# Kernel optimization log

Hardware: AMD Instinct MI355X
Metric: run time of the kernel (lower is better)

Reference implementation:

```python
import jax, jax.numpy as jnp
import numpy as np

N_NODES = 100000


def setup_inputs() -> dict:
    key = jax.random.key(0)
    k1, k2, k3, k4, k5, k6 = jax.random.split(key, 6)
    x = jax.random.normal(k1, (N_NODES, 256), dtype=jnp.float32)
    edge_index = jax.random.randint(k2, (2, 3200000), 0, N_NODES, dtype=jnp.int64)
    # GCNConv(256, 3): glorot weight + zero bias (PyG default)
    lim1 = float(np.sqrt(6.0 / (256 + 3)))
    W1 = jax.random.uniform(k3, (256, 3), minval=-lim1, maxval=lim1, dtype=jnp.float32)
    b1 = jnp.zeros((3,), dtype=jnp.float32)
    # Linear(3, 7): torch default kaiming-uniform-ish bounds
    lim2 = float(1.0 / np.sqrt(3))
    W2 = jax.random.uniform(k4, (3, 7), minval=-lim2, maxval=lim2, dtype=jnp.float32)
    b2 = jax.random.uniform(k5, (7,), minval=-lim2, maxval=lim2, dtype=jnp.float32)
    return {"x": x, "edge_index": edge_index, "W1": W1, "b1": b1, "W2": W2, "b2": b2}


def gcn_conv(x, edge_index, W, b, num_nodes):
    # PyG GCNConv: add self-loops, symmetric deg^-1/2 (A+I) deg^-1/2 normalization,
    # aggregate transformed features, then add bias.
    loop = jnp.arange(num_nodes, dtype=edge_index.dtype)
    src = jnp.concatenate([edge_index[0], loop])
    dst = jnp.concatenate([edge_index[1], loop])
    ones = jnp.ones_like(dst, dtype=x.dtype)
    deg = jax.ops.segment_sum(ones, dst, num_segments=num_nodes)  # [N]
    dinv = jnp.where(deg > 0, jax.lax.rsqrt(deg), 0.0)
    norm = dinv[src] * dinv[dst]  # [E+N]
    h = x @ W  # [N, 3] — transform BEFORE gather (small width)
    msg = h[src] * norm[:, None]  # [E+N, 3]
    agg = jax.ops.segment_sum(msg, dst, num_segments=num_nodes)  # [N, 3]
    return agg + b


def reference(x, edge_index, W1, b1, W2, b2):
    h = jax.nn.relu(gcn_conv(x, edge_index, W1, b1, x.shape[0]))  # [N, 3]
    z = h @ W2 + b2  # [N, 7]
    return (h, z)
```

## Files before the change

kernel.cpp:

```cpp
#include <hip/hip_runtime.h>
#include <stdint.h>


#define BSHIFT 8
#define BNODES 256

__global__ void k_detect(const unsigned* __restrict__ ei, int* __restrict__ flag) {
    if (blockIdx.x == 0 && threadIdx.x == 0) {
        int is64 = 1;
        for (int i = 1; i < 512; i += 2)
            if (ei[i] != 0u) { is64 = 0; break; }
        *flag = is64;
    }
}

__global__ __launch_bounds__(256) void k_xw1(const float* __restrict__ x,
                                             const float* __restrict__ W1,
                                             float* __restrict__ hpre4,
                                             unsigned* __restrict__ zptr,
                                             int nzero_words, int N) {
    const int gtid    = blockIdx.x * 256 + threadIdx.x;
    const int nthread = gridDim.x * 256;
    for (int i = gtid; i < nzero_words; i += nthread) zptr[i] = 0u;

    const int lane = threadIdx.x & 63;
    float w[4][3];
#pragma unroll
    for (int k = 0; k < 4; ++k)
#pragma unroll
        for (int c = 0; c < 3; ++c)
            w[k][c] = W1[(lane * 4 + k) * 3 + c];

    const int wave   = gtid >> 6;
    const int nwaves = nthread >> 6;
    for (int node = wave; node < N; node += nwaves) {
        const float4 v = *reinterpret_cast<const float4*>(x + (size_t)node * 256 + lane * 4);
        float s0 = v.x * w[0][0] + v.y * w[1][0] + v.z * w[2][0] + v.w * w[3][0];
        float s1 = v.x * w[0][1] + v.y * w[1][1] + v.z * w[2][1] + v.w * w[3][1];
        float s2 = v.x * w[0][2] + v.y * w[1][2] + v.z * w[2][2] + v.w * w[3][2];
#pragma unroll
        for (int off = 32; off > 0; off >>= 1) {
            s0 += __shfl_xor(s0, off, 64);
            s1 += __shfl_xor(s1, off, 64);
            s2 += __shfl_xor(s2, off, 64);
        }
        if (lane == 0)
            reinterpret_cast<float4*>(hpre4)[node] = make_float4(s0, s1, s2, 0.f);
    }
}

__global__ __launch_bounds__(512) void k_bin(const unsigned* __restrict__ ei,
                                             const int* __restrict__ flag,
                                             unsigned* __restrict__ gcount,
                                             unsigned* __restrict__ records,
                                             unsigned* __restrict__ ovf_cnt,
                                             unsigned* __restrict__ ovf,
                                             int E, int B, int CAP, int OVFCAP, int CH) {
    __shared__ unsigned cnt[512], base[512], cursor[512];
    const int e0 = blockIdx.x * CH;
    const int e1 = min(E, e0 + CH);
    for (int i = threadIdx.x; i < B; i += 512) { cnt[i] = 0u; cursor[i] = 0u; }
    __syncthreads();
    const bool is64 = (*flag != 0);
    const unsigned long long* e64 = (const unsigned long long*)ei;
    for (int e = e0 + threadIdx.x; e < e1; e += 512) {
        const unsigned d = is64 ? (unsigned)e64[(size_t)E + e] : ei[(size_t)E + e];
        atomicAdd(&cnt[d >> BSHIFT], 1u);
    }
    __syncthreads();
    for (int i = threadIdx.x; i < B; i += 512)
        base[i] = cnt[i] ? atomicAdd(&gcount[i], cnt[i]) : 0u;
    __syncthreads();
    for (int e = e0 + threadIdx.x; e < e1; e += 512) {
        unsigned s, d;
        if (is64) {
            s = (unsigned)e64[e];
            d = (unsigned)e64[(size_t)E + e];
        } else {
            s = ei[e];
            d = ei[(size_t)E + e];
        }
        const unsigned bb  = d >> BSHIFT;
        const unsigned idx = base[bb] + atomicAdd(&cursor[bb], 1u);
        if (idx < (unsigned)CAP) {
            records[(size_t)bb * CAP + idx] = (s << BSHIFT) | (d & (BNODES - 1));
        } else {
            const unsigned o = atomicAdd(ovf_cnt, 1u);
            if (o < (unsigned)OVFCAP) { ovf[2 * o] = s; ovf[2 * o + 1] = d; }
        }
    }
}

__global__ __launch_bounds__(256) void k_count(const unsigned* __restrict__ gcount,
                                               const unsigned* __restrict__ records,
                                               const unsigned* __restrict__ ovf_cnt,
                                               const unsigned* __restrict__ ovf,
                                               float* __restrict__ g4,
                                               int N, int CAP, int OVFCAP) {
    __shared__ unsigned cnt[BNODES];
    const int b = blockIdx.x;
    cnt[threadIdx.x] = 0u;
    __syncthreads();
    const unsigned n = min(gcount[b], (unsigned)CAP);
    const unsigned* rec = records + (size_t)b * CAP;
    for (unsigned i = threadIdx.x; i < n; i += 256)
        atomicAdd(&cnt[rec[i] & (BNODES - 1)], 1u);
    const unsigned no = min(*ovf_cnt, (unsigned)OVFCAP);
    for (unsigned i = threadIdx.x; i < no; i += 256) {
        const unsigned d = ovf[2 * i + 1];
        if ((int)(d >> BSHIFT) == b) atomicAdd(&cnt[d & (BNODES - 1)], 1u);
    }
    __syncthreads();
    const int node = (b << BSHIFT) + threadIdx.x;
    if (node < N) {
        const float r = rsqrtf(1.0f + (float)cnt[threadIdx.x]);
        const float4 h = reinterpret_cast<const float4*>(g4)[node];
        reinterpret_cast<float4*>(g4)[node] = make_float4(h.x * r, h.y * r, h.z * r, r);
    }
}

__global__ __launch_bounds__(256) void k_msg(const unsigned* __restrict__ gcount,
                                             const unsigned* __restrict__ records,
                                             const unsigned* __restrict__ ovf_cnt,
                                             const unsigned* __restrict__ ovf,
                                             const float* __restrict__ g4,
                                             const float* __restrict__ b1,
                                             const float* __restrict__ W2,
                                             const float* __restrict__ b2,
                                             float* __restrict__ out,
                                             int N, int CAP, int OVFCAP) {
    __shared__ float acc[BNODES * 3];
    const int b = blockIdx.x;
    for (int i = threadIdx.x; i < BNODES * 3; i += 256) acc[i] = 0.f;
    __syncthreads();
    const unsigned n = min(gcount[b], (unsigned)CAP);
    const unsigned* rec = records + (size_t)b * CAP;
    for (unsigned i = threadIdx.x; i < n; i += 256) {
        const unsigned r   = rec[i];
        const unsigned low = r & (BNODES - 1);
        const float4   g   = reinterpret_cast<const float4*>(g4)[r >> BSHIFT];
        atomicAdd(&acc[low * 3 + 0], g.x);
        atomicAdd(&acc[low * 3 + 1], g.y);
        atomicAdd(&acc[low * 3 + 2], g.z);
    }
    const unsigned no = min(*ovf_cnt, (unsigned)OVFCAP);
    for (unsigned i = threadIdx.x; i < no; i += 256) {
        const unsigned d = ovf[2 * i + 1];
        if ((int)(d >> BSHIFT) == b) {
            const unsigned low = d & (BNODES - 1);
            const float4   g   = reinterpret_cast<const float4*>(g4)[ovf[2 * i]];
            atomicAdd(&acc[low * 3 + 0], g.x);
            atomicAdd(&acc[low * 3 + 1], g.y);
            atomicAdd(&acc[low * 3 + 2], g.z);
        }
    }
    __syncthreads();
    const int node = (b << BSHIFT) + threadIdx.x;
    if (node < N) {
        const float4 gs = reinterpret_cast<const float4*>(g4)[node];
        const float  r  = gs.w;
        const int    t  = threadIdx.x;
        const float h0 = fmaxf(r * (acc[t * 3 + 0] + gs.x) + b1[0], 0.f);
        const float h1 = fmaxf(r * (acc[t * 3 + 1] + gs.y) + b1[1], 0.f);
        const float h2 = fmaxf(r * (acc[t * 3 + 2] + gs.z) + b1[2], 0.f);
        out[3 * (size_t)node + 0] = h0;
        out[3 * (size_t)node + 1] = h1;
        out[3 * (size_t)node + 2] = h2;
        float* z = out + (size_t)3 * N;
#pragma unroll
        for (int c = 0; c < 7; ++c)
            z[7 * (size_t)node + c] = h0 * W2[c] + h1 * W2[7 + c] + h2 * W2[14 + c] + b2[c];
    }
}

__global__ __launch_bounds__(256) void k_deg_fb(const unsigned* __restrict__ ei,
                                                const int* __restrict__ flag,
                                                float* __restrict__ deg, int E) {
    const int e = blockIdx.x * 256 + threadIdx.x;
    if (e >= E) return;
    const unsigned d = (*flag) ? (unsigned)((const unsigned long long*)ei)[(size_t)E + e]
                               : ei[(size_t)E + e];
    atomicAdd(&deg[d], 1.0f);
}
__global__ __launch_bounds__(256) void k_dinv_fb(const float* __restrict__ deg,
                                                 float* __restrict__ g4, int N) {
    const int i = blockIdx.x * 256 + threadIdx.x;
    if (i >= N) return;
    const float r = rsqrtf(1.0f + deg[i]);
    const float4 h = reinterpret_cast<const float4*>(g4)[i];
    reinterpret_cast<float4*>(g4)[i] = make_float4(h.x * r, h.y * r, h.z * r, r);
}
__global__ __launch_bounds__(256) void k_edge_fb(const unsigned* __restrict__ ei,
                                                 const int* __restrict__ flag,
                                                 const float* __restrict__ g4,
                                                 float* __restrict__ u4, int E) {
    const int e = blockIdx.x * 256 + threadIdx.x;
    if (e >= E) return;
    unsigned s, d;
    if (*flag) {
        const unsigned long long* q = (const unsigned long long*)ei;
        s = (unsigned)q[e];
        d = (unsigned)q[(size_t)E + e];
    } else {
        s = ei[e];
        d = ei[(size_t)E + e];
    }
    const float4 g = reinterpret_cast<const float4*>(g4)[s];
    atomicAdd(&u4[4 * (size_t)d + 0], g.x);
    atomicAdd(&u4[4 * (size_t)d + 1], g.y);
    atomicAdd(&u4[4 * (size_t)d + 2], g.z);
}
__global__ __launch_bounds__(256) void k_final_fb(const float* __restrict__ u4,
                                                  const float* __restrict__ g4,
                                                  const float* __restrict__ b1,
                                                  const float* __restrict__ W2,
                                                  const float* __restrict__ b2,
                                                  float* __restrict__ out, int N) {
    const int i = blockIdx.x * 256 + threadIdx.x;
    if (i >= N) return;
    const float4 gs = reinterpret_cast<const float4*>(g4)[i];
    const float4 u  = reinterpret_cast<const float4*>(u4)[i];
    const float  r  = gs.w;
    const float h0 = fmaxf(r * (u.x + gs.x) + b1[0], 0.f);
    const float h1 = fmaxf(r * (u.y + gs.y) + b1[1], 0.f);
    const float h2 = fmaxf(r * (u.z + gs.z) + b1[2], 0.f);
    out[3 * (size_t)i + 0] = h0;
    out[3 * (size_t)i + 1] = h1;
    out[3 * (size_t)i + 2] = h2;
    float* z = out + (size_t)3 * N;
#pragma unroll
    for (int c = 0; c < 7; ++c)
        z[7 * (size_t)i + c] = h0 * W2[c] + h1 * W2[7 + c] + h2 * W2[14 + c] + b2[c];
}

extern "C" void kernel_launch(void* const* d_in, const int* in_sizes, int n_in,
                              void* d_out, int out_size, void* d_ws, size_t ws_size,
                              hipStream_t stream) {
    const float*    x   = (const float*)d_in[0];
    const unsigned* ei  = (const unsigned*)d_in[1];
    const float*    W1  = (const float*)d_in[2];
    const float*    b1  = (const float*)d_in[3];
    const float*    W2  = (const float*)d_in[4];
    const float*    b2  = (const float*)d_in[5];
    float*          out = (float*)d_out;

    const int N = in_sizes[0] / 256;
    const int E = in_sizes[1] / 2;
    const int B = (N + BNODES - 1) >> BSHIFT;

    char*     ws      = (char*)d_ws;
    int*      flag    = (int*)ws;
    unsigned* gcount  = (unsigned*)(ws + 256);
    unsigned* ovf_cnt = gcount + B;
    size_t    off     = (256 + 4 * (size_t)(B + 1) + 255) & ~(size_t)255;
    float*    g4      = (float*)(ws + off);
    off += 16 * (size_t)N;
    off  = (off + 255) & ~(size_t)255;

    const int OVFCAP = 1 << 16;
    size_t rec_off = off;
    size_t avail   = (ws_size > rec_off + 8 * (size_t)OVFCAP + 4096)
                       ? ws_size - rec_off - 8 * (size_t)OVFCAP - 4096 : 0;
    int CAP = (int)((avail / (4 * (size_t)B)) > 16384 ? 16384 : (avail / (4 * (size_t)B)));
    const bool binned = (CAP >= 8960);

    k_detect<<<1, 64, 0, stream>>>(ei, flag);

    if (binned) {
        unsigned* records = (unsigned*)(ws + rec_off);
        unsigned* ovf     = records + (size_t)B * CAP;
        const int CH      = 16384;
        const int nbin    = (E + CH - 1) / CH;
        k_xw1<<<4096, 256, 0, stream>>>(x, W1, g4, gcount, B + 1, N);
        k_bin<<<nbin, 512, 0, stream>>>(ei, flag, gcount, records, ovf_cnt, ovf,
                                        E, B, CAP, OVFCAP, CH);
        k_count<<<B, 256, 0, stream>>>(gcount, records, ovf_cnt, ovf, g4, N, CAP, OVFCAP);
        k_msg<<<B, 256, 0, stream>>>(gcount, records, ovf_cnt, ovf, g4,
                                     b1, W2, b2, out, N, CAP, OVFCAP);
    } else {
        float* deg = (float*)(ws + rec_off);
        float* u4  = deg + N;
        k_xw1<<<4096, 256, 0, stream>>>(x, W1, g4, (unsigned*)deg, 5 * N, N);
        k_deg_fb<<<(E + 255) / 256, 256, 0, stream>>>(ei, flag, deg, E);
        k_dinv_fb<<<(N + 255) / 256, 256, 0, stream>>>(deg, g4, N);
        k_edge_fb<<<(E + 255) / 256, 256, 0, stream>>>(ei, flag, g4, u4, E);
        k_final_fb<<<(N + 255) / 256, 256, 0, stream>>>(u4, g4, b1, W2, b2, out, N);
    }
}
```

Measured before the change: 142.5 us.

## Split per-bin count and message passes across blocks, fuse XW1 with edge binning

Merges the x@W1 projection and the edge binning into one launch, with disjoint block ranges doing each job so they run concurrently. The separate int64-detection kernel is dropped, and each block now detects the index width itself with a syncthreads_or. The per-bin degree-count and message-aggregation kernels are each split into SPLIT slices per bin, which writes partial results that new small kernels reduce. This gives many more blocks than the roughly 391 bins, at the cost of extra partial-buffer traffic and two more launches.

```diff
diff --git a/kernel.cpp b/kernel.cpp
--- a/kernel.cpp
+++ b/kernel.cpp
@@ -4,35 +4,219 @@
 
 #define BSHIFT 8
 #define BNODES 256
-
-__global__ void k_detect(const unsigned* __restrict__ ei, int* __restrict__ flag) {
-    if (blockIdx.x == 0 && threadIdx.x == 0) {
-        int is64 = 1;
-        for (int i = 1; i < 512; i += 2)
-            if (ei[i] != 0u) { is64 = 0; break; }
-        *flag = is64;
-    }
-}
-
-__global__ __launch_bounds__(256) void k_xw1(const float* __restrict__ x,
+#define OVFCAP 32768
+
+__device__ __forceinline__ bool ei_is64(const unsigned* __restrict__ ei) {
+    const int t = threadIdx.x;
+    const int nz = (t < 256) && (ei[2 * t + 1] != 0u);
+    return __syncthreads_or(nz) == 0;
+}
+
+__global__ __launch_bounds__(512) void k_pre(const float* __restrict__ x,
                                              const float* __restrict__ W1,
-                                             float* __restrict__ hpre4,
-                                             unsigned* __restrict__ zptr,
-                                             int nzero_words, int N) {
-    const int gtid    = blockIdx.x * 256 + threadIdx.x;
+                                             float* __restrict__ g4,
+                                             const unsigned* __restrict__ ei,
+                                             unsigned* __restrict__ gcount,
+                                             unsigned* __restrict__ records,
+                                             unsigned* __restrict__ ovf,
+                                             int E, int B, int CAP, int CH,
+                                             int nbin, int N) {
+    const bool is64 = ei_is64(ei);
+    if ((int)blockIdx.x < nbin) {
+        __shared__ unsigned cnt[512], base[512], cursor[512];
+        const int e0 = blockIdx.x * CH;
+        const int e1 = min(E, e0 + CH);
+        for (int i = threadIdx.x; i < B; i += 512) { cnt[i] = 0u; cursor[i] = 0u; }
+        __syncthreads();
+        const unsigned long long* e64 = (const unsigned long long*)ei;
+        for (int e = e0 + threadIdx.x; e < e1; e += 512) {
+            const unsigned d = is64 ? (unsigned)e64[(size_t)E + e] : ei[(size_t)E + e];
+            atomicAdd(&cnt[d >> BSHIFT], 1u);
+        }
+        __syncthreads();
+        for (int i = threadIdx.x; i < B; i += 512)
+            base[i] = cnt[i] ? atomicAdd(&gcount[i], cnt[i]) : 0u;
+        __syncthreads();
+        unsigned* ovf_cnt = gcount + B;
+        for (int e = e0 + threadIdx.x; e < e1; e += 512) {
+            unsigned s, d;
+            if (is64) { s = (unsigned)e64[e]; d = (unsigned)e64[(size_t)E + e]; }
+            else      { s = ei[e];            d = ei[(size_t)E + e]; }
+            const unsigned bb  = d >> BSHIFT;
+            const unsigned idx = base[bb] + atomicAdd(&cursor[bb], 1u);
+            if (idx < (unsigned)CAP) {
+                records[(size_t)bb * CAP + idx] = (s << BSHIFT) | (d & (BNODES - 1));
+            } else {
+                const unsigned o = atomicAdd(ovf_cnt, 1u);
+                if (o < (unsigned)OVFCAP) { ovf[2 * o] = s; ovf[2 * o + 1] = d; }
+            }
+        }
+    } else {
+        const int bx      = blockIdx.x - nbin;
+        const int gtid    = bx * 512 + threadIdx.x;
+        const int nthread = ((int)gridDim.x - nbin) * 512;
+        const int lane    = threadIdx.x & 63;
+        float w[4][3];
+#pragma unroll
+        for (int k = 0; k < 4; ++k)
+#pragma unroll
+            for (int c = 0; c < 3; ++c)
+                w[k][c] = W1[(lane * 4 + k) * 3 + c];
+        const int wave   = gtid >> 6;
+        const int nwaves = nthread >> 6;
+        for (int node = wave; node < N; node += nwaves) {
+            const float4 v = *reinterpret_cast<const float4*>(x + (size_t)node * 256 + lane * 4);
+            float s0 = v.x * w[0][0] + v.y * w[1][0] + v.z * w[2][0] + v.w * w[3][0];
+            float s1 = v.x * w[0][1] + v.y * w[1][1] + v.z * w[2][1] + v.w * w[3][1];
+            float s2 = v.x * w[0][2] + v.y * w[1][2] + v.z * w[2][2] + v.w * w[3][2];
+#pragma unroll
+            for (int off = 32; off > 0; off >>= 1) {
+                s0 += __shfl_xor(s0, off, 64);
+                s1 += __shfl_xor(s1, off, 64);
+                s2 += __shfl_xor(s2, off, 64);
+            }
+            if (lane == 0)
+                reinterpret_cast<float4*>(g4)[node] = make_float4(s0, s1, s2, 0.f);
+        }
+    }
+}
+
+__global__ __launch_bounds__(256) void k_cnt2(const unsigned* __restrict__ gcount,
+                                              const unsigned* __restrict__ records,
+                                              const unsigned* __restrict__ ovf,
+                                              unsigned* __restrict__ pcount,
+                                              int B, int CAP, int SPLIT) {
+    __shared__ unsigned cnt[BNODES];
+    const int b  = blockIdx.x / SPLIT;
+    const int sl = blockIdx.x - b * SPLIT;
+    cnt[threadIdx.x] = 0u;
+    __syncthreads();
+    unsigned n = gcount[b]; if (n > (unsigned)CAP) n = CAP;
+    const unsigned chunk = (n + SPLIT - 1) / SPLIT;
+    const unsigned lo = sl * chunk;
+    const unsigned hi = (lo + chunk < n) ? lo + chunk : n;
+    const unsigned* rec = records + (size_t)b * CAP;
+    for (unsigned i = lo + threadIdx.x; i < hi; i += 256)
+        atomicAdd(&cnt[rec[i] & (BNODES - 1)], 1u);
+    if (sl == 0) {
+        unsigned no = gcount[B]; if (no > (unsigned)OVFCAP) no = OVFCAP;
+        for (unsigned i = threadIdx.x; i < no; i += 256) {
+            const unsigned d = ovf[2 * i + 1];
+            if ((int)(d >> BSHIFT) == b) atomicAdd(&cnt[d & (BNODES - 1)], 1u);
+        }
+    }
+    __syncthreads();
+    pcount[((size_t)blockIdx.x << BSHIFT) + threadIdx.x] = cnt[threadIdx.x];
+}
+
+__global__ __launch_bounds__(256) void k_dinv2(const unsigned* __restrict__ pcount,
+                                               float* __restrict__ g4, int N, int SPLIT) {
+    const int i = blockIdx.x * 256 + threadIdx.x;
+    if (i >= N) return;
+    const int b = i >> BSHIFT, t = i & (BNODES - 1);
+    unsigned deg = 1u;
+    for (int s = 0; s < SPLIT; ++s)
+        deg += pcount[(((size_t)b * SPLIT + s) << BSHIFT) + t];
+    const float r = rsqrtf((float)deg);
+    const float4 h = reinterpret_cast<const float4*>(g4)[i];
+    reinterpret_cast<float4*>(g4)[i] = make_float4(h.x * r, h.y * r, h.z * r, r);
+}
+
+__global__ __launch_bounds__(256) void k_msg2(const unsigned* __restrict__ gcount,
+                                              const unsigned* __restrict__ records,
+                                              const unsigned* __restrict__ ovf,
+                                              const float* __restrict__ g4,
+                                              float* __restrict__ psum,
+                                              int B, int CAP, int SPLIT) {
+    __shared__ float acc[BNODES * 3];
+    const int b  = blockIdx.x / SPLIT;
+    const int sl = blockIdx.x - b * SPLIT;
+    for (int i = threadIdx.x; i < BNODES * 3; i += 256) acc[i] = 0.f;
+    __syncthreads();
+    unsigned n = gcount[b]; if (n > (unsigned)CAP) n = CAP;
+    const unsigned chunk = (n + SPLIT - 1) / SPLIT;
+    const unsigned lo = sl * chunk;
+    const unsigned hi = (lo + chunk < n) ? lo + chunk : n;
+    const unsigned* rec = records + (size_t)b * CAP;
+    const float4* g4v = reinterpret_cast<const float4*>(g4);
+    unsigned i = lo + threadIdx.x;
+    for (; i + 256 < hi; i += 512) {
+        const unsigned r0 = rec[i], r1 = rec[i + 256];
+        const float4 ga = g4v[r0 >> BSHIFT];
+        const float4 gb = g4v[r1 >> BSHIFT];
+        const unsigned l0 = (r0 & (BNODES - 1)) * 3, l1 = (r1 & (BNODES - 1)) * 3;
+        atomicAdd(&acc[l0 + 0], ga.x); atomicAdd(&acc[l0 + 1], ga.y); atomicAdd(&acc[l0 + 2], ga.z);
+        atomicAdd(&acc[l1 + 0], gb.x); atomicAdd(&acc[l1 + 1], gb.y); atomicAdd(&acc[l1 + 2], gb.z);
+    }
+    if (i < hi) {
+        const unsigned r0 = rec[i];
+        const float4 ga = g4v[r0 >> BSHIFT];
+        const unsigned l0 = (r0 & (BNODES - 1)) * 3;
+        atomicAdd(&acc[l0 + 0], ga.x); atomicAdd(&acc[l0 + 1], ga.y); atomicAdd(&acc[l0 + 2], ga.z);
+    }
+    if (sl == 0) {
+        unsigned no = gcount[B]; if (no > (unsigned)OVFCAP) no = OVFCAP;
+        for (unsigned k = threadIdx.x; k < no; k += 256) {
+            const unsigned d = ovf[2 * k + 1];
+            if ((int)(d >> BSHIFT) == b) {
+                const float4 g = g4v[ovf[2 * k]];
+                const unsigned l = (d & (BNODES - 1)) * 3;
+                atomicAdd(&acc[l + 0], g.x); atomicAdd(&acc[l + 1], g.y); atomicAdd(&acc[l + 2], g.z);
+            }
+        }
+    }
+    __syncthreads();
+    const size_t base = ((size_t)blockIdx.x * 3) << BSHIFT;
+    psum[base +   0 + threadIdx.x] = acc[threadIdx.x * 3 + 0];
+    psum[base + 256 + threadIdx.x] = acc[threadIdx.x * 3 + 1];
+    psum[base + 512 + threadIdx.x] = acc[threadIdx.x * 3 + 2];
+}
+
+__global__ __launch_bounds__(256) void k_fin(const float* __restrict__ psum,
+                                             const float* __restrict__ g4,
+                                             const float* __restrict__ b1,
+                                             const float* __restrict__ W2,
+                                             const float* __restrict__ b2,
+                                             float* __restrict__ out, int N, int SPLIT) {
+    const int i = blockIdx.x * 256 + threadIdx.x;
+    if (i >= N) return;
+    const int b = i >> BSHIFT, t = i & (BNODES - 1);
+    float a0 = 0.f, a1 = 0.f, a2 = 0.f;
+    for (int s = 0; s < SPLIT; ++s) {
+        const size_t base = (((size_t)b * SPLIT + s) * 3) << BSHIFT;
+        a0 += psum[base + t];
+        a1 += psum[base + 256 + t];
+        a2 += psum[base + 512 + t];
+    }
+    const float4 g = reinterpret_cast<const float4*>(g4)[i];
+    const float  r = g.w;
+    const float h0 = fmaxf(r * (a0 + g.x) + b1[0], 0.f);
+    const float h1 = fmaxf(r * (a1 + g.y) + b1[1], 0.f);
+    const float h2 = fmaxf(r * (a2 + g.z) + b1[2], 0.f);
+    out[3 * (size_t)i + 0] = h0;
+    out[3 * (size_t)i + 1] = h1;
+    out[3 * (size_t)i + 2] = h2;
+    float* z = out + (size_t)3 * N;
+#pragma unroll
+    for (int c = 0; c < 7; ++c)
+        z[7 * (size_t)i + c] = h0 * W2[c] + h1 * W2[7 + c] + h2 * W2[14 + c] + b2[c];
+}
+
+__global__ __launch_bounds__(256) void k_xw1_fb(const float* __restrict__ x,
+                                                const float* __restrict__ W1,
+                                                float* __restrict__ g4,
+                                                unsigned* __restrict__ zptr,
+                                                int nzero, int N) {
+    const int gtid = blockIdx.x * 256 + threadIdx.x;
     const int nthread = gridDim.x * 256;
-    for (int i = gtid; i < nzero_words; i += nthread) zptr[i] = 0u;
-
+    for (int i = gtid; i < nzero; i += nthread) zptr[i] = 0u;
     const int lane = threadIdx.x & 63;
     float w[4][3];
 #pragma unroll
     for (int k = 0; k < 4; ++k)
 #pragma unroll
-        for (int c = 0; c < 3; ++c)
-            w[k][c] = W1[(lane * 4 + k) * 3 + c];
-
-    const int wave   = gtid >> 6;
-    const int nwaves = nthread >> 6;
+        for (int c = 0; c < 3; ++c) w[k][c] = W1[(lane * 4 + k) * 3 + c];
+    const int wave = gtid >> 6, nwaves = nthread >> 6;
     for (int node = wave; node < N; node += nwaves) {
         const float4 v = *reinterpret_cast<const float4*>(x + (size_t)node * 256 + lane * 4);
         float s0 = v.x * w[0][0] + v.y * w[1][0] + v.z * w[2][0] + v.w * w[3][0];
@@ -45,141 +229,16 @@
             s2 += __shfl_xor(s2, off, 64);
         }
         if (lane == 0)
-            reinterpret_cast<float4*>(hpre4)[node] = make_float4(s0, s1, s2, 0.f);
-    }
-}
-
-__global__ __launch_bounds__(512) void k_bin(const unsigned* __restrict__ ei,
-                                             const int* __restrict__ flag,
-                                             unsigned* __restrict__ gcount,
-                                             unsigned* __restrict__ records,
-                                             unsigned* __restrict__ ovf_cnt,
-                                             unsigned* __restrict__ ovf,
-                                             int E, int B, int CAP, int OVFCAP, int CH) {
-    __shared__ unsigned cnt[512], base[512], cursor[512];
-    const int e0 = blockIdx.x * CH;
-    const int e1 = min(E, e0 + CH);
-    for (int i = threadIdx.x; i < B; i += 512) { cnt[i] = 0u; cursor[i] = 0u; }
-    __syncthreads();
-    const bool is64 = (*flag != 0);
-    const unsigned long long* e64 = (const unsigned long long*)ei;
-    for (int e = e0 + threadIdx.x; e < e1; e += 512) {
-        const unsigned d = is64 ? (unsigned)e64[(size_t)E + e] : ei[(size_t)E + e];
-        atomicAdd(&cnt[d >> BSHIFT], 1u);
-    }
-    __syncthreads();
-    for (int i = threadIdx.x; i < B; i += 512)
-        base[i] = cnt[i] ? atomicAdd(&gcount[i], cnt[i]) : 0u;
-    __syncthreads();
-    for (int e = e0 + threadIdx.x; e < e1; e += 512) {
-        unsigned s, d;
-        if (is64) {
-            s = (unsigned)e64[e];
-            d = (unsigned)e64[(size_t)E + e];
-        } else {
-            s = ei[e];
-            d = ei[(size_t)E + e];
-        }
-        const unsigned bb  = d >> BSHIFT;
-        const unsigned idx = base[bb] + atomicAdd(&cursor[bb], 1u);
-        if (idx < (unsigned)CAP) {
-            records[(size_t)bb * CAP + idx] = (s << BSHIFT) | (d & (BNODES - 1));
-        } else {
-            const unsigned o = atomicAdd(ovf_cnt, 1u);
-            if (o < (unsigned)OVFCAP) { ovf[2 * o] = s; ovf[2 * o + 1] = d; }
-        }
-    }
-}
-
-__global__ __launch_bounds__(256) void k_count(const unsigned* __restrict__ gcount,
-                                               const unsigned* __restrict__ records,
-                                               const unsigned* __restrict__ ovf_cnt,
-                                               const unsigned* __restrict__ ovf,
-                                               float* __restrict__ g4,
-                                               int N, int CAP, int OVFCAP) {
-    __shared__ unsigned cnt[BNODES];
-    const int b = blockIdx.x;
-    cnt[threadIdx.x] = 0u;
-    __syncthreads();
-    const unsigned n = min(gcount[b], (unsigned)CAP);
-    const unsigned* rec = records + (size_t)b * CAP;
-    for (unsigned i = threadIdx.x; i < n; i += 256)
-        atomicAdd(&cnt[rec[i] & (BNODES - 1)], 1u);
-    const unsigned no = min(*ovf_cnt, (unsigned)OVFCAP);
-    for (unsigned i = threadIdx.x; i < no; i += 256) {
-        const unsigned d = ovf[2 * i + 1];
-        if ((int)(d >> BSHIFT) == b) atomicAdd(&cnt[d & (BNODES - 1)], 1u);
-    }
-    __syncthreads();
-    const int node = (b << BSHIFT) + threadIdx.x;
-    if (node < N) {
-        const float r = rsqrtf(1.0f + (float)cnt[threadIdx.x]);
-        const float4 h = reinterpret_cast<const float4*>(g4)[node];
-        reinterpret_cast<float4*>(g4)[node] = make_float4(h.x * r, h.y * r, h.z * r, r);
-    }
-}
-
-__global__ __launch_bounds__(256) void k_msg(const unsigned* __restrict__ gcount,
-                                             const unsigned* __restrict__ records,
-                                             const unsigned* __restrict__ ovf_cnt,
-                                             const unsigned* __restrict__ ovf,
-                                             const float* __restrict__ g4,
-                                             const float* __restrict__ b1,
-                                             const float* __restrict__ W2,
-                                             const float* __restrict__ b2,
-                                             float* __restrict__ out,
-                                             int N, int CAP, int OVFCAP) {
-    __shared__ float acc[BNODES * 3];
-    const int b = blockIdx.x;
-    for (int i = threadIdx.x; i < BNODES * 3; i += 256) acc[i] = 0.f;
-    __syncthreads();
-    const unsigned n = min(gcount[b], (unsigned)CAP);
-    const unsigned* rec = records + (size_t)b * CAP;
-    for (unsigned i = threadIdx.x; i < n; i += 256) {
-        const unsigned r   = rec[i];
-        const unsigned low = r & (BNODES - 1);
-        const float4   g   = reinterpret_cast<const float4*>(g4)[r >> BSHIFT];
-        atomicAdd(&acc[low * 3 + 0], g.x);
-        atomicAdd(&acc[low * 3 + 1], g.y);
-        atomicAdd(&acc[low * 3 + 2], g.z);
-    }
-    const unsigned no = min(*ovf_cnt, (unsigned)OVFCAP);
-    for (unsigned i = threadIdx.x; i < no; i += 256) {
-        const unsigned d = ovf[2 * i + 1];
-        if ((int)(d >> BSHIFT) == b) {
-            const unsigned low = d & (BNODES - 1);
-            const float4   g   = reinterpret_cast<const float4*>(g4)[ovf[2 * i]];
-            atomicAdd(&acc[low * 3 + 0], g.x);
-            atomicAdd(&acc[low * 3 + 1], g.y);
-            atomicAdd(&acc[low * 3 + 2], g.z);
-        }
-    }
-    __syncthreads();
-    const int node = (b << BSHIFT) + threadIdx.x;
-    if (node < N) {
-        const float4 gs = reinterpret_cast<const float4*>(g4)[node];
-        const float  r  = gs.w;
-        const int    t  = threadIdx.x;
-        const float h0 = fmaxf(r * (acc[t * 3 + 0] + gs.x) + b1[0], 0.f);
-        const float h1 = fmaxf(r * (acc[t * 3 + 1] + gs.y) + b1[1], 0.f);
-        const float h2 = fmaxf(r * (acc[t * 3 + 2] + gs.z) + b1[2], 0.f);
-        out[3 * (size_t)node + 0] = h0;
-        out[3 * (size_t)node + 1] = h1;
-        out[3 * (size_t)node + 2] = h2;
-        float* z = out + (size_t)3 * N;
-#pragma unroll
-        for (int c = 0; c < 7; ++c)
-            z[7 * (size_t)node + c] = h0 * W2[c] + h1 * W2[7 + c] + h2 * W2[14 + c] + b2[c];
-    }
-}
-
+            reinterpret_cast<float4*>(g4)[node] = make_float4(s0, s1, s2, 0.f);
+    }
+}
 __global__ __launch_bounds__(256) void k_deg_fb(const unsigned* __restrict__ ei,
-                                                const int* __restrict__ flag,
                                                 float* __restrict__ deg, int E) {
+    const bool is64 = ei_is64(ei);
     const int e = blockIdx.x * 256 + threadIdx.x;
     if (e >= E) return;
-    const unsigned d = (*flag) ? (unsigned)((const unsigned long long*)ei)[(size_t)E + e]
-                               : ei[(size_t)E + e];
+    const unsigned d = is64 ? (unsigned)((const unsigned long long*)ei)[(size_t)E + e]
+                            : ei[(size_t)E + e];
     atomicAdd(&deg[d], 1.0f);
 }
 __global__ __launch_bounds__(256) void k_dinv_fb(const float* __restrict__ deg,
@@ -191,19 +250,17 @@
     reinterpret_cast<float4*>(g4)[i] = make_float4(h.x * r, h.y * r, h.z * r, r);
 }
 __global__ __launch_bounds__(256) void k_edge_fb(const unsigned* __restrict__ ei,
-                                                 const int* __restrict__ flag,
                                                  const float* __restrict__ g4,
                                                  float* __restrict__ u4, int E) {
+    const bool is64 = ei_is64(ei);
     const int e = blockIdx.x * 256 + threadIdx.x;
     if (e >= E) return;
     unsigned s, d;
-    if (*flag) {
+    if (is64) {
         const unsigned long long* q = (const unsigned long long*)ei;
-        s = (unsigned)q[e];
-        d = (unsigned)q[(size_t)E + e];
+        s = (unsigned)q[e]; d = (unsigned)q[(size_t)E + e];
     } else {
-        s = ei[e];
-        d = ei[(size_t)E + e];
+        s = ei[e]; d = ei[(size_t)E + e];
     }
     const float4 g = reinterpret_cast<const float4*>(g4)[s];
     atomicAdd(&u4[4 * (size_t)d + 0], g.x);
@@ -218,12 +275,12 @@
                                                   float* __restrict__ out, int N) {
     const int i = blockIdx.x * 256 + threadIdx.x;
     if (i >= N) return;
-    const float4 gs = reinterpret_cast<const float4*>(g4)[i];
-    const float4 u  = reinterpret_cast<const float4*>(u4)[i];
-    const float  r  = gs.w;
-    const float h0 = fmaxf(r * (u.x + gs.x) + b1[0], 0.f);
-    const float h1 = fmaxf(r * (u.y + gs.y) + b1[1], 0.f);
-    const float h2 = fmaxf(r * (u.z + gs.z) + b1[2], 0.f);
+    const float4 g = reinterpret_cast<const float4*>(g4)[i];
+    const float4 u = reinterpret_cast<const float4*>(u4)[i];
+    const float  r = g.w;
+    const float h0 = fmaxf(r * (u.x + g.x) + b1[0], 0.f);
+    const float h1 = fmaxf(r * (u.y + g.y) + b1[1], 0.f);
+    const float h2 = fmaxf(r * (u.z + g.z) + b1[2], 0.f);
     out[3 * (size_t)i + 0] = h0;
     out[3 * (size_t)i + 1] = h1;
     out[3 * (size_t)i + 2] = h2;
@@ -248,42 +305,48 @@
     const int E = in_sizes[1] / 2;
     const int B = (N + BNODES - 1) >> BSHIFT;
 
-    char*     ws      = (char*)d_ws;
-    int*      flag    = (int*)ws;
-    unsigned* gcount  = (unsigned*)(ws + 256);
-    unsigned* ovf_cnt = gcount + B;
-    size_t    off     = (256 + 4 * (size_t)(B + 1) + 255) & ~(size_t)255;
-    float*    g4      = (float*)(ws + off);
-    off += 16 * (size_t)N;
-    off  = (off + 255) & ~(size_t)255;
-
-    const int OVFCAP = 1 << 16;
-    size_t rec_off = off;
-    size_t avail   = (ws_size > rec_off + 8 * (size_t)OVFCAP + 4096)
-                       ? ws_size - rec_off - 8 * (size_t)OVFCAP - 4096 : 0;
-    int CAP = (int)((avail / (4 * (size_t)B)) > 16384 ? 16384 : (avail / (4 * (size_t)B)));
-    const bool binned = (CAP >= 8960);
-
-    k_detect<<<1, 64, 0, stream>>>(ei, flag);
-
-    if (binned) {
+    char*     ws     = (char*)d_ws;
+    unsigned* gcount = (unsigned*)ws;
+    size_t off = (4ull * (B + 1) + 255) & ~(size_t)255;
+    float*    g4  = (float*)(ws + off);
+    off = (off + 16ull * N + 255) & ~(size_t)255;
+    unsigned* ovf = (unsigned*)(ws + off);
+    off = (off + 8ull * OVFCAP + 255) & ~(size_t)255;
+    const size_t puoff = off;
+
+    int SPLIT = 0, CAP = 0;
+    size_t rec_off = 0;
+    const int sps[4] = {8, 4, 2, 1};
+    for (int si = 0; si < 4; ++si) {
+        const int sp = sps[si];
+        const size_t ro = (puoff + 4ull * B * sp * 768 + 255) & ~(size_t)255;
+        if (ws_size < ro + 4096) continue;
+        long cap = (long)((ws_size - ro) / (4ull * B));
+        if (cap > 12288) cap = 12288;
+        if (cap >= 8960) { SPLIT = sp; CAP = (int)cap; rec_off = ro; break; }
+    }
+
+    if (SPLIT) {
+        unsigned* pcount  = (unsigned*)(ws + puoff);
+        float*    psum    = (float*)(ws + puoff);
         unsigned* records = (unsigned*)(ws + rec_off);
-        unsigned* ovf     = records + (size_t)B * CAP;
-        const int CH      = 16384;
-        const int nbin    = (E + CH - 1) / CH;
-        k_xw1<<<4096, 256, 0, stream>>>(x, W1, g4, gcount, B + 1, N);
-        k_bin<<<nbin, 512, 0, stream>>>(ei, flag, gcount, records, ovf_cnt, ovf,
-                                        E, B, CAP, OVFCAP, CH);
-        k_count<<<B, 256, 0, stream>>>(gcount, records, ovf_cnt, ovf, g4, N, CAP, OVFCAP);
-        k_msg<<<B, 256, 0, stream>>>(gcount, records, ovf_cnt, ovf, g4,
-                                     b1, W2, b2, out, N, CAP, OVFCAP);
+        hipMemsetAsync(gcount, 0, 4ull * (B + 1), stream);
+        const int CH   = 16384;
+        const int nbin = (E + CH - 1) / CH;
+        const int NBX  = 2048;
+        k_pre<<<nbin + NBX, 512, 0, stream>>>(x, W1, g4, ei, gcount, records, ovf,
+                                              E, B, CAP, CH, nbin, N);
+        k_cnt2<<<B * SPLIT, 256, 0, stream>>>(gcount, records, ovf, pcount, B, CAP, SPLIT);
+        k_dinv2<<<(N + 255) / 256, 256, 0, stream>>>(pcount, g4, N, SPLIT);
+        k_msg2<<<B * SPLIT, 256, 0, stream>>>(gcount, records, ovf, g4, psum, B, CAP, SPLIT);
+        k_fin<<<(N + 255) / 256, 256, 0, stream>>>(psum, g4, b1, W2, b2, out, N, SPLIT);
     } else {
-        float* deg = (float*)(ws + rec_off);
+        float* deg = (float*)(ws + puoff);
         float* u4  = deg + N;
-        k_xw1<<<4096, 256, 0, stream>>>(x, W1, g4, (unsigned*)deg, 5 * N, N);
-        k_deg_fb<<<(E + 255) / 256, 256, 0, stream>>>(ei, flag, deg, E);
+        k_xw1_fb<<<4096, 256, 0, stream>>>(x, W1, g4, (unsigned*)deg, 5 * N, N);
+        k_deg_fb<<<(E + 255) / 256, 256, 0, stream>>>(ei, deg, E);
         k_dinv_fb<<<(N + 255) / 256, 256, 0, stream>>>(deg, g4, N);
-        k_edge_fb<<<(E + 255) / 256, 256, 0, stream>>>(ei, flag, g4, u4, E);
+        k_edge_fb<<<(E + 255) / 256, 256, 0, stream>>>(ei, g4, u4, E);
         k_final_fb<<<(N + 255) / 256, 256, 0, stream>>>(u4, g4, b1, W2, b2, out, N);
     }
 }
```

Measured after the change: 118.4 us. 16.9% less time.
